# Performance work log

Hardware: AMD Instinct MI355X
Metric: run time of the kernel (lower is better)

Reference implementation:

```python
import jax, jax.numpy as jnp
import numpy as np

N_HEADS = 16

def setup_inputs() -> dict:
    key = jax.random.key(0)
    k1, k2, k3 = jax.random.split(key, 3)
    d = 1024
    x = jax.random.normal(k1, (2, 2048, d), dtype=jnp.float32)
    W_in = jax.random.normal(k2, (d, 3 * d), dtype=jnp.float32) * (d ** -0.5)
    W_out = jax.random.normal(k3, (d, d), dtype=jnp.float32) * (d ** -0.5)
    return {"x": x, "W_in": W_in, "W_out": W_out}

def reference(x, W_in, W_out):
    B, S, D = x.shape
    H = N_HEADS
    Dh = D // H
    qkv = x @ W_in                                  # [B,S,3D]
    q, k, v = jnp.split(qkv, 3, axis=-1)
    # [B,S,D] -> [B,H,S,Dh]
    q = q.reshape(B, S, H, Dh).transpose(0, 2, 1, 3)
    k = k.reshape(B, S, H, Dh).transpose(0, 2, 1, 3)
    v = v.reshape(B, S, H, Dh).transpose(0, 2, 1, 3)
    scores = jnp.einsum('bhqd,bhkd->bhqk', q, k)    # [B,H,S,S]
    causal = jnp.triu(jnp.ones((S, S), dtype=bool), k=1)
    scores = jnp.where(causal, -jnp.inf, scores)
    scores = scores / jnp.sqrt(jnp.asarray(Dh, scores.dtype))
    attn = jax.nn.softmax(scores, axis=-1)
    out = jnp.einsum('bhqk,bhkd->bhqd', attn, v)    # [B,H,S,Dh]
    out = out.transpose(0, 2, 1, 3).reshape(B, S, D)
    return out @ W_out
```

## Files before the change

### kernel.cpp

```cpp
#include <hip/hip_runtime.h>
#include <cstdint>
#include <cstddef>

typedef __bf16 bf16;
typedef bf16  bf16x4  __attribute__((ext_vector_type(4)));
typedef bf16  bf16x8  __attribute__((ext_vector_type(8)));
typedef float floatx4 __attribute__((ext_vector_type(4)));

#define BATCH 2
#define SEQ   2048
#define DIM   1024
#define NH    16
#define DH    64
#define D3    3072
#define MROWS 4096

__device__ __forceinline__ void gld16(void* lds, const void* gptr) {
  __builtin_amdgcn_global_load_lds(
      (const __attribute__((address_space(1))) unsigned int*)gptr,
      (__attribute__((address_space(3))) unsigned int*)lds, 16, 0, 0);
}

__global__ __launch_bounds__(256) void k_prep(const float4* __restrict__ x,
                                              bf16* __restrict__ xb,
                                              const float* __restrict__ Wi,
                                              bf16* __restrict__ wti,
                                              const float* __restrict__ Wo,
                                              bf16* __restrict__ wto) {
  __shared__ float tile[32][33];
  const int bid = blockIdx.x;
  if (bid < 4096) {
    int i = bid * 256 + threadIdx.x;
    float4 v = x[i];
    bf16x4 o;
    o.x = (bf16)v.x; o.y = (bf16)v.y; o.z = (bf16)v.z; o.w = (bf16)v.w;
    *(bf16x4*)(xb + (size_t)i * 4) = o;
    return;
  }
  const float* W; bf16* Wt; int N, id;
  if (bid < 7168) { W = Wi; Wt = wti; N = 3072; id = bid - 4096; }
  else            { W = Wo; Wt = wto; N = 1024; id = bid - 7168; }
  const int nb = N / 32;
  int n0 = (id % nb) * 32, k0 = (id / nb) * 32;
  int tx = threadIdx.x & 31, ty = threadIdx.x >> 5;
#pragma unroll
  for (int i = 0; i < 4; i++)
    tile[ty + i * 8][tx] = W[(size_t)(k0 + ty + i * 8) * N + n0 + tx];
  __syncthreads();
#pragma unroll
  for (int i = 0; i < 4; i++)
    Wt[(size_t)(n0 + ty + i * 8) * 1024 + k0 + tx] = (bf16)tile[tx][ty + i * 8];
}

template <typename OutT, int MODE, int BN>
__global__ __launch_bounds__(256) void k_gemm_bt(const bf16* __restrict__ A,
                                                 const bf16* __restrict__ Bt,
                                                 OutT* __restrict__ C,
                                                 bf16* __restrict__ qk,
                                                 bf16* __restrict__ vt,
                                                 int M, int N, int K) {
  constexpr int LN = 2 + BN / 64;
  __shared__ __align__(16) bf16 As[3][128 * 32];
  __shared__ __align__(16) bf16 Bs[3][BN * 32];
  const int t = threadIdx.x, l = t & 63, w = t >> 6;
  const int q = l >> 4, mm = l & 15;
  const int m0 = blockIdx.y * 128, n0 = blockIdx.x * BN;
  constexpr int MT = (BN == 128) ? 4 : 2;
  const int mo = (BN == 128) ? ((w >> 1) * 64) : (w * 32);
  const int no = (BN == 128) ? ((w & 1) * 64) : 0;
  const int sw = (mm >> 1) & 3;

  auto stage = [&](int kt) {
    const int bp = kt % 3;
#pragma unroll
    for (int i = 0; i < 2; i++) {
      int c = t + i * 256;
      int row = c >> 2, pos = c & 3;
      int gs = pos ^ ((row >> 1) & 3);
      gld16((char*)As[bp] + (size_t)c * 16, A + (size_t)(m0 + row) * K + kt * 32 + gs * 8);
    }
#pragma unroll
    for (int i = 0; i < BN / 64; i++) {
      int c = t + i * 256;
      int row = c >> 2, pos = c & 3;
      int gs = pos ^ ((row >> 1) & 3);
      gld16((char*)Bs[bp] + (size_t)c * 16, Bt + (size_t)(n0 + row) * K + kt * 32 + gs * 8);
    }
  };

  floatx4 acc[MT][4] = {};
  const int nk = K >> 5;

  stage(0);
  stage(1);

  for (int kt = 0; kt < nk; kt++) {
    if (kt + 1 < nk)
      asm volatile("s_waitcnt vmcnt(%0)\n\ts_barrier" :: "n"(LN) : "memory");
    else
      asm volatile("s_waitcnt vmcnt(0)\n\ts_barrier" ::: "memory");
    if (kt + 2 < nk) stage(kt + 2);

    const bf16* Ab = As[kt % 3];
    const bf16* Bb = Bs[kt % 3];
    bf16x8 af[MT], bfr[4];
#pragma unroll
    for (int mt = 0; mt < MT; mt++)
      af[mt] = *(const bf16x8*)(Ab + (size_t)(mo + mt * 16 + mm) * 32 + (q ^ sw) * 8);
#pragma unroll
    for (int nt = 0; nt < 4; nt++)
      bfr[nt] = *(const bf16x8*)(Bb + (size_t)(no + nt * 16 + mm) * 32 + (q ^ sw) * 8);
#pragma unroll
    for (int mt = 0; mt < MT; mt++)
#pragma unroll
      for (int nt = 0; nt < 4; nt++)
        acc[mt][nt] = __builtin_amdgcn_mfma_f32_16x16x32_bf16(af[mt], bfr[nt],
                                                              acc[mt][nt], 0, 0, 0);
  }
#pragma unroll
  for (int mt = 0; mt < MT; mt++)
#pragma unroll
    for (int nt = 0; nt < 4; nt++)
#pragma unroll
      for (int r = 0; r < 4; r++) {
        int row = m0 + mo + mt * 16 + q * 4 + r;
        int col = n0 + no + nt * 16 + mm;
        if (MODE == 0) {
          C[(size_t)row * N + col] = (OutT)acc[mt][nt][r];
        } else {
          if (col < 2048) {
            qk[(size_t)row * 2048 + col] = (bf16)acc[mt][nt][r];
          } else {
            int d = col - 2048;
            int hh = d >> 6, dh = d & 63;
            int bb = row >> 11, s = row & 2047;
            vt[((size_t)(bb * 16 + hh) * 64 + dh) * SEQ + s] = (bf16)acc[mt][nt][r];
          }
        }
      }
}

__global__ __launch_bounds__(256, 4) void k_attn(const bf16* __restrict__ qk,
                                                 const bf16* __restrict__ vt,
                                                 bf16* __restrict__ out) {
  const int bx = blockIdx.x;
  const int qt = 31 - (bx >> 5);
  const int bh = bx & 31;
  const int b = bh >> 4, h = bh & 15;
  const int t = threadIdx.x, l = t & 63, w = t >> 6;
  const int q4 = l >> 4, mm = l & 15;
  const int sw = (mm >> 1) & 3;

  __shared__ __align__(16) char lds[8192 + 16384 + 16384];
  bf16* Qs = (bf16*)lds;
  bf16* Ps = (bf16*)lds;
  bf16* Ks = (bf16*)(lds + 8192);
  bf16* Vs = (bf16*)(lds + 8192 + 16384);

  const size_t qkbase = (size_t)b * SEQ * 2048;
  const size_t vtbase = (size_t)bh * 64 * SEQ;

  auto stage = [&](int kt) {
    const int bp = kt & 1;
#pragma unroll
    for (int i = 0; i < 2; i++) {
      int row = t >> 2, pos = t & 3;
      int g = pos ^ ((row >> 1) & 3);
      gld16((char*)(Ks + bp * 4096) + ((size_t)t + i * 256) * 16,
            qk + qkbase + (size_t)(kt * 64 + row) * 2048 + 1024 + h * 64 + i * 32 + g * 8);
    }
#pragma unroll
    for (int i = 0; i < 2; i++) {
      int c = t + i * 256;
      int vr = c >> 3, vc = c & 7;
      int src = vc ^ (vr & 7);
      gld16((char*)(Vs + bp * 4096) + (size_t)c * 16,
            vt + vtbase + (size_t)vr * SEQ + kt * 64 + src * 8);
    }
  };

  {
    int row = t >> 2, col = (t & 3) * 8;
#pragma unroll
    for (int i = 0; i < 2; i++)
      gld16((char*)Qs + ((size_t)t + i * 256) * 16,
            qk + qkbase + (size_t)(qt * 64 + row) * 2048 + h * 64 + i * 32 + col);
  }
  stage(0);
  __syncthreads();
  bf16x8 qf[2];
#pragma unroll
  for (int ks = 0; ks < 2; ks++) {
    qf[ks] = *(const bf16x8*)(Qs + (size_t)(ks * 64 + w * 16 + mm) * 32 + q4 * 8);
#pragma unroll
    for (int j = 0; j < 8; j++)
      qf[ks][j] = (bf16)((float)qf[ks][j] * 0.18033688f);
  }
  __syncthreads();

  float l_i = 0.f;
  floatx4 oaccT[4] = {};
  const int qloc = w * 16 + mm;
  const float FM = 24.0f;

  bf16* Pw = Ps + (size_t)w * 640;

  for (int kt = 0; kt <= qt; kt++) {
    if (kt < qt) stage(kt + 1);
    const bf16* Kb = Ks + (kt & 1) * 4096;
    const bf16* Vb = Vs + (kt & 1) * 4096;

    floatx4 sacc[4] = {};
#pragma unroll
    for (int ks = 0; ks < 2; ks++)
#pragma unroll
      for (int ct = 0; ct < 4; ct++) {
        bf16x8 kf = *(const bf16x8*)(Kb + (size_t)(ks * 64 + ct * 16 + mm) * 32 + (q4 ^ sw) * 8);
        sacc[ct] = __builtin_amdgcn_mfma_f32_16x16x32_bf16(kf, qf[ks], sacc[ct], 0, 0, 0);
      }

    bf16x4 pk[4];
    float rsum = 0.f;
    if (kt == qt) {
#pragma unroll
      for (int ct = 0; ct < 4; ct++)
#pragma unroll
        for (int r = 0; r < 4; r++) {
          float e = (ct * 16 + q4 * 4 + r > qloc)
                        ? 0.f : __builtin_amdgcn_exp2f(sacc[ct][r] - FM);
          pk[ct][r] = (bf16)e;
          rsum += e;
        }
    } else {
#pragma unroll
      for (int ct = 0; ct < 4; ct++)
#pragma unroll
        for (int r = 0; r < 4; r++) {
          float e = __builtin_amdgcn_exp2f(sacc[ct][r] - FM);
          pk[ct][r] = (bf16)e;
          rsum += e;
        }
    }
    rsum += __shfl_xor(rsum, 16, 64);
    rsum += __shfl_xor(rsum, 32, 64);
    l_i += rsum;

#pragma unroll
    for (int ks = 0; ks < 2; ks++) {
      *(bf16x4*)(Pw + (size_t)mm * 40 + q4 * 4)      = pk[ks * 2 + 0];
      *(bf16x4*)(Pw + (size_t)mm * 40 + 16 + q4 * 4) = pk[ks * 2 + 1];
      bf16x8 pf = *(const bf16x8*)(Pw + (size_t)mm * 40 + q4 * 8);
#pragma unroll
      for (int nt = 0; nt < 4; nt++) {
        int chunk = (ks * 4 + q4) ^ (mm & 7);
        bf16x8 vf = *(const bf16x8*)(Vb + (size_t)(nt * 16 + mm) * 64 + chunk * 8);
        oaccT[nt] = __builtin_amdgcn_mfma_f32_16x16x32_bf16(vf, pf, oaccT[nt], 0, 0, 0);
      }
    }

    if (kt < qt) __syncthreads();
  }

  float inv = 1.0f / l_i;
  int qrow = qt * 64 + qloc;
  bf16* orow = out + ((size_t)b * SEQ + qrow) * DIM + h * 64;
#pragma unroll
  for (int nt = 0; nt < 4; nt++) {
    bf16x4 o4;
#pragma unroll
    for (int r = 0; r < 4; r++) o4[r] = (bf16)(oaccT[nt][r] * inv);
    *(bf16x4*)(orow + nt * 16 + q4 * 4) = o4;
  }
}

extern "C" void kernel_launch(void* const* d_in, const int* in_sizes, int n_in,
                              void* d_out, int out_size, void* d_ws, size_t ws_size,
                              hipStream_t stream) {
  const float* x     = (const float*)d_in[0];
  const float* W_in  = (const float*)d_in[1];
  const float* W_out = (const float*)d_in[2];
  float* out = (float*)d_out;

  char* ws = (char*)d_ws;
  bf16* xb   = (bf16*)(ws);
  bf16* wti  = (bf16*)(ws + 8388608);
  bf16* wto  = (bf16*)(ws + 14680064);
  bf16* qkb  = (bf16*)(ws + 16777216);
  bf16* vtb  = (bf16*)(ws + 33554432);
  bf16* attn = xb;

  k_prep<<<8192, 256, 0, stream>>>((const float4*)x, xb, W_in, wti, W_out, wto);
  k_gemm_bt<bf16, 1, 128><<<dim3(24, 32), 256, 0, stream>>>(xb, wti, nullptr, qkb, vtb,
                                                            MROWS, D3, DIM);
  k_attn<<<1024, 256, 0, stream>>>(qkb, vtb, attn);
  k_gemm_bt<float, 0, 64><<<dim3(16, 32), 256, 0, stream>>>(attn, wto, out, nullptr, nullptr,
                                                            MROWS, DIM, DIM);
}
```

Before: 175.1 us.

## Split attention KV loop across warps and retile output projection GEMM

The attention kernel now gives each of the four warps a strided subset of key tiles for all 64 query rows, instead of giving each warp 16 query rows over every key tile. K and V fragments are loaded straight from global memory into registers, which removes the LDS staging and the per-iteration block barriers. Partial outputs and row sums are combined through LDS at the end. This uses more registers (occupancy hint drops from 4 to 2), adds a reduction step, and leaves load imbalance across warps on short causal rows. Separately, the GEMM is generalized to a BM parameter, and the output projection uses 64x64 tiles with twice as many blocks.

```diff
diff --git a/kernel.cpp b/kernel.cpp
--- a/kernel.cpp
+++ b/kernel.cpp
@@ -52,28 +52,28 @@
     Wt[(size_t)(n0 + ty + i * 8) * 1024 + k0 + tx] = (bf16)tile[tx][ty + i * 8];
 }
 
-template <typename OutT, int MODE, int BN>
+template <typename OutT, int MODE, int BM, int BN>
 __global__ __launch_bounds__(256) void k_gemm_bt(const bf16* __restrict__ A,
                                                  const bf16* __restrict__ Bt,
                                                  OutT* __restrict__ C,
                                                  bf16* __restrict__ qk,
                                                  bf16* __restrict__ vt,
                                                  int M, int N, int K) {
-  constexpr int LN = 2 + BN / 64;
-  __shared__ __align__(16) bf16 As[3][128 * 32];
+  constexpr int LN = BM / 64 + BN / 64;
+  constexpr int MT = BM / 32, NT = BN / 32;
+  __shared__ __align__(16) bf16 As[3][BM * 32];
   __shared__ __align__(16) bf16 Bs[3][BN * 32];
   const int t = threadIdx.x, l = t & 63, w = t >> 6;
   const int q = l >> 4, mm = l & 15;
-  const int m0 = blockIdx.y * 128, n0 = blockIdx.x * BN;
-  constexpr int MT = (BN == 128) ? 4 : 2;
-  const int mo = (BN == 128) ? ((w >> 1) * 64) : (w * 32);
-  const int no = (BN == 128) ? ((w & 1) * 64) : 0;
+  const int m0 = blockIdx.y * BM, n0 = blockIdx.x * BN;
+  const int mo = (w >> 1) * (BM / 2);
+  const int no = (w & 1) * (BN / 2);
   const int sw = (mm >> 1) & 3;
 
   auto stage = [&](int kt) {
     const int bp = kt % 3;
 #pragma unroll
-    for (int i = 0; i < 2; i++) {
+    for (int i = 0; i < BM / 64; i++) {
       int c = t + i * 256;
       int row = c >> 2, pos = c & 3;
       int gs = pos ^ ((row >> 1) & 3);
@@ -88,7 +88,7 @@
     }
   };
 
-  floatx4 acc[MT][4] = {};
+  floatx4 acc[MT][NT] = {};
   const int nk = K >> 5;
 
   stage(0);
@@ -103,24 +103,24 @@
 
     const bf16* Ab = As[kt % 3];
     const bf16* Bb = Bs[kt % 3];
-    bf16x8 af[MT], bfr[4];
+    bf16x8 af[MT], bfr[NT];
 #pragma unroll
     for (int mt = 0; mt < MT; mt++)
       af[mt] = *(const bf16x8*)(Ab + (size_t)(mo + mt * 16 + mm) * 32 + (q ^ sw) * 8);
 #pragma unroll
-    for (int nt = 0; nt < 4; nt++)
+    for (int nt = 0; nt < NT; nt++)
       bfr[nt] = *(const bf16x8*)(Bb + (size_t)(no + nt * 16 + mm) * 32 + (q ^ sw) * 8);
 #pragma unroll
     for (int mt = 0; mt < MT; mt++)
 #pragma unroll
-      for (int nt = 0; nt < 4; nt++)
+      for (int nt = 0; nt < NT; nt++)
         acc[mt][nt] = __builtin_amdgcn_mfma_f32_16x16x32_bf16(af[mt], bfr[nt],
                                                               acc[mt][nt], 0, 0, 0);
   }
 #pragma unroll
   for (int mt = 0; mt < MT; mt++)
 #pragma unroll
-    for (int nt = 0; nt < 4; nt++)
+    for (int nt = 0; nt < NT; nt++)
 #pragma unroll
       for (int r = 0; r < 4; r++) {
         int row = m0 + mo + mt * 16 + q * 4 + r;
@@ -140,7 +140,7 @@
       }
 }
 
-__global__ __launch_bounds__(256, 4) void k_attn(const bf16* __restrict__ qk,
+__global__ __launch_bounds__(256, 2) void k_attn(const bf16* __restrict__ qk,
                                                  const bf16* __restrict__ vt,
                                                  bf16* __restrict__ out) {
   const int bx = blockIdx.x;
@@ -149,35 +149,16 @@
   const int b = bh >> 4, h = bh & 15;
   const int t = threadIdx.x, l = t & 63, w = t >> 6;
   const int q4 = l >> 4, mm = l & 15;
-  const int sw = (mm >> 1) & 3;
-
-  __shared__ __align__(16) char lds[8192 + 16384 + 16384];
-  bf16* Qs = (bf16*)lds;
-  bf16* Ps = (bf16*)lds;
-  bf16* Ks = (bf16*)(lds + 8192);
-  bf16* Vs = (bf16*)(lds + 8192 + 16384);
+
+  __shared__ __align__(16) char lds[5120 + 66560 + 1024];
+  bf16*  Ps    = (bf16*)lds;
+  bf16*  Qs    = (bf16*)(lds + 5120);
+  float* Opart = (float*)(lds + 5120);
+  float* Lpart = (float*)(lds + 5120 + 66560);
 
   const size_t qkbase = (size_t)b * SEQ * 2048;
-  const size_t vtbase = (size_t)bh * 64 * SEQ;
-
-  auto stage = [&](int kt) {
-    const int bp = kt & 1;
-#pragma unroll
-    for (int i = 0; i < 2; i++) {
-      int row = t >> 2, pos = t & 3;
-      int g = pos ^ ((row >> 1) & 3);
-      gld16((char*)(Ks + bp * 4096) + ((size_t)t + i * 256) * 16,
-            qk + qkbase + (size_t)(kt * 64 + row) * 2048 + 1024 + h * 64 + i * 32 + g * 8);
-    }
-#pragma unroll
-    for (int i = 0; i < 2; i++) {
-      int c = t + i * 256;
-      int vr = c >> 3, vc = c & 7;
-      int src = vc ^ (vr & 7);
-      gld16((char*)(Vs + bp * 4096) + (size_t)c * 16,
-            vt + vtbase + (size_t)vr * SEQ + kt * 64 + src * 8);
-    }
-  };
+  const bf16* kb = qk + qkbase + 1024 + h * 64;
+  const bf16* vb = vt + (size_t)bh * 64 * SEQ;
 
   {
     int row = t >> 2, col = (t & 3) * 8;
@@ -186,90 +167,110 @@
       gld16((char*)Qs + ((size_t)t + i * 256) * 16,
             qk + qkbase + (size_t)(qt * 64 + row) * 2048 + h * 64 + i * 32 + col);
   }
-  stage(0);
-  __syncthreads();
-  bf16x8 qf[2];
-#pragma unroll
-  for (int ks = 0; ks < 2; ks++) {
-    qf[ks] = *(const bf16x8*)(Qs + (size_t)(ks * 64 + w * 16 + mm) * 32 + q4 * 8);
-#pragma unroll
-    for (int j = 0; j < 8; j++)
-      qf[ks][j] = (bf16)((float)qf[ks][j] * 0.18033688f);
-  }
-  __syncthreads();
-
-  float l_i = 0.f;
-  floatx4 oaccT[4] = {};
-  const int qloc = w * 16 + mm;
+  __syncthreads();
+  bf16x8 qf[4][2];
+#pragma unroll
+  for (int g = 0; g < 4; g++)
+#pragma unroll
+    for (int ks = 0; ks < 2; ks++) {
+      qf[g][ks] = *(const bf16x8*)(Qs + (size_t)(ks * 64 + g * 16 + mm) * 32 + q4 * 8);
+#pragma unroll
+      for (int j = 0; j < 8; j++)
+        qf[g][ks][j] = (bf16)((float)qf[g][ks][j] * 0.18033688f);
+    }
+  __syncthreads();
+
+  float l_i[4] = {0.f, 0.f, 0.f, 0.f};
+  floatx4 oacc[4][4] = {};
   const float FM = 24.0f;
-
   bf16* Pw = Ps + (size_t)w * 640;
 
-  for (int kt = 0; kt <= qt; kt++) {
-    if (kt < qt) stage(kt + 1);
-    const bf16* Kb = Ks + (kt & 1) * 4096;
-    const bf16* Vb = Vs + (kt & 1) * 4096;
-
-    floatx4 sacc[4] = {};
+  for (int kt = w; kt <= qt; kt += 4) {
+    bf16x8 kf[2][4], vf[2][4];
 #pragma unroll
     for (int ks = 0; ks < 2; ks++)
 #pragma unroll
-      for (int ct = 0; ct < 4; ct++) {
-        bf16x8 kf = *(const bf16x8*)(Kb + (size_t)(ks * 64 + ct * 16 + mm) * 32 + (q4 ^ sw) * 8);
-        sacc[ct] = __builtin_amdgcn_mfma_f32_16x16x32_bf16(kf, qf[ks], sacc[ct], 0, 0, 0);
+      for (int ct = 0; ct < 4; ct++)
+        kf[ks][ct] = *(const bf16x8*)(kb + (size_t)(kt * 64 + ct * 16 + mm) * 2048 +
+                                      ks * 32 + q4 * 8);
+#pragma unroll
+    for (int ks = 0; ks < 2; ks++)
+#pragma unroll
+      for (int nt = 0; nt < 4; nt++)
+        vf[ks][nt] = *(const bf16x8*)(vb + (size_t)(nt * 16 + mm) * 2048 +
+                                      kt * 64 + ks * 32 + q4 * 8);
+    const bool diag = (kt == qt);
+
+#pragma unroll
+    for (int g = 0; g < 4; g++) {
+      floatx4 sacc[4] = {};
+#pragma unroll
+      for (int ks = 0; ks < 2; ks++)
+#pragma unroll
+        for (int ct = 0; ct < 4; ct++)
+          sacc[ct] = __builtin_amdgcn_mfma_f32_16x16x32_bf16(kf[ks][ct], qf[g][ks],
+                                                             sacc[ct], 0, 0, 0);
+      bf16x4 pk[4];
+      float rsum = 0.f;
+      const int qloc = g * 16 + mm;
+      if (diag) {
+#pragma unroll
+        for (int ct = 0; ct < 4; ct++)
+#pragma unroll
+          for (int r = 0; r < 4; r++) {
+            float e = (ct * 16 + q4 * 4 + r > qloc)
+                          ? 0.f : __builtin_amdgcn_exp2f(sacc[ct][r] - FM);
+            pk[ct][r] = (bf16)e;
+            rsum += e;
+          }
+      } else {
+#pragma unroll
+        for (int ct = 0; ct < 4; ct++)
+#pragma unroll
+          for (int r = 0; r < 4; r++) {
+            float e = __builtin_amdgcn_exp2f(sacc[ct][r] - FM);
+            pk[ct][r] = (bf16)e;
+            rsum += e;
+          }
       }
-
-    bf16x4 pk[4];
-    float rsum = 0.f;
-    if (kt == qt) {
-#pragma unroll
-      for (int ct = 0; ct < 4; ct++)
-#pragma unroll
-        for (int r = 0; r < 4; r++) {
-          float e = (ct * 16 + q4 * 4 + r > qloc)
-                        ? 0.f : __builtin_amdgcn_exp2f(sacc[ct][r] - FM);
-          pk[ct][r] = (bf16)e;
-          rsum += e;
-        }
-    } else {
-#pragma unroll
-      for (int ct = 0; ct < 4; ct++)
-#pragma unroll
-        for (int r = 0; r < 4; r++) {
-          float e = __builtin_amdgcn_exp2f(sacc[ct][r] - FM);
-          pk[ct][r] = (bf16)e;
-          rsum += e;
-        }
-    }
-    rsum += __shfl_xor(rsum, 16, 64);
-    rsum += __shfl_xor(rsum, 32, 64);
-    l_i += rsum;
-
-#pragma unroll
-    for (int ks = 0; ks < 2; ks++) {
-      *(bf16x4*)(Pw + (size_t)mm * 40 + q4 * 4)      = pk[ks * 2 + 0];
-      *(bf16x4*)(Pw + (size_t)mm * 40 + 16 + q4 * 4) = pk[ks * 2 + 1];
-      bf16x8 pf = *(const bf16x8*)(Pw + (size_t)mm * 40 + q4 * 8);
-#pragma unroll
-      for (int nt = 0; nt < 4; nt++) {
-        int chunk = (ks * 4 + q4) ^ (mm & 7);
-        bf16x8 vf = *(const bf16x8*)(Vb + (size_t)(nt * 16 + mm) * 64 + chunk * 8);
-        oaccT[nt] = __builtin_amdgcn_mfma_f32_16x16x32_bf16(vf, pf, oaccT[nt], 0, 0, 0);
+      rsum += __shfl_xor(rsum, 16, 64);
+      rsum += __shfl_xor(rsum, 32, 64);
+      l_i[g] += rsum;
+
+#pragma unroll
+      for (int ks = 0; ks < 2; ks++) {
+        *(bf16x4*)(Pw + (size_t)mm * 40 + q4 * 4)      = pk[ks * 2 + 0];
+        *(bf16x4*)(Pw + (size_t)mm * 40 + 16 + q4 * 4) = pk[ks * 2 + 1];
+        bf16x8 pf = *(const bf16x8*)(Pw + (size_t)mm * 40 + q4 * 8);
+#pragma unroll
+        for (int nt = 0; nt < 4; nt++)
+          oacc[g][nt] = __builtin_amdgcn_mfma_f32_16x16x32_bf16(vf[ks][nt], pf,
+                                                                oacc[g][nt], 0, 0, 0);
       }
     }
-
-    if (kt < qt) __syncthreads();
-  }
-
-  float inv = 1.0f / l_i;
-  int qrow = qt * 64 + qloc;
-  bf16* orow = out + ((size_t)b * SEQ + qrow) * DIM + h * 64;
-#pragma unroll
-  for (int nt = 0; nt < 4; nt++) {
-    bf16x4 o4;
-#pragma unroll
-    for (int r = 0; r < 4; r++) o4[r] = (bf16)(oaccT[nt][r] * inv);
-    *(bf16x4*)(orow + nt * 16 + q4 * 4) = o4;
+  }
+
+#pragma unroll
+  for (int g = 0; g < 4; g++) {
+#pragma unroll
+    for (int nt = 0; nt < 4; nt++)
+#pragma unroll
+      for (int r = 0; r < 4; r++)
+        Opart[(size_t)w * 4160 + (nt * 16 + q4 * 4 + r) * 65 + g * 16 + mm] = oacc[g][nt][r];
+    if (q4 == 0) Lpart[w * 64 + g * 16 + mm] = l_i[g];
+  }
+  __syncthreads();
+
+  {
+    const int d = t & 63, qb = (t >> 6) * 16;
+#pragma unroll
+    for (int i = 0; i < 16; i++) {
+      int qq = qb + i;
+      float lsum = Lpart[qq] + Lpart[64 + qq] + Lpart[128 + qq] + Lpart[192 + qq];
+      float v = Opart[(size_t)d * 65 + qq] + Opart[4160 + (size_t)d * 65 + qq] +
+                Opart[8320 + (size_t)d * 65 + qq] + Opart[12480 + (size_t)d * 65 + qq];
+      out[((size_t)b * SEQ + qt * 64 + qq) * DIM + h * 64 + d] = (bf16)(v / lsum);
+    }
   }
 }
 
@@ -290,9 +291,9 @@
   bf16* attn = xb;
 
   k_prep<<<8192, 256, 0, stream>>>((const float4*)x, xb, W_in, wti, W_out, wto);
-  k_gemm_bt<bf16, 1, 128><<<dim3(24, 32), 256, 0, stream>>>(xb, wti, nullptr, qkb, vtb,
-                                                            MROWS, D3, DIM);
+  k_gemm_bt<bf16, 1, 128, 128><<<dim3(24, 32), 256, 0, stream>>>(xb, wti, nullptr, qkb, vtb,
+                                                                 MROWS, D3, DIM);
   k_attn<<<1024, 256, 0, stream>>>(qkb, vtb, attn);
-  k_gemm_bt<float, 0, 64><<<dim3(16, 32), 256, 0, stream>>>(attn, wto, out, nullptr, nullptr,
-                                                            MROWS, DIM, DIM);
-}
+  k_gemm_bt<float, 0, 64, 64><<<dim3(16, 64), 256, 0, stream>>>(attn, wto, out, nullptr, nullptr,
+                                                                MROWS, DIM, DIM);
+}
```

After: 185.3 us. 1.06x slower.
